# Kernel optimization log

Measured on AMD Instinct MI355X. Metric: run time of the kernel, lower is better.

Reference implementation:

```python
import jax, jax.numpy as jnp
import numpy as np

D_EMBED = 1024
N_HEADS = 16
D_HEAD = 64
D_MLP = 4096
SEQ = 2048
BATCH = 2
ALPHA = 1.0


def setup_inputs() -> dict:
    key = jax.random.key(0)
    ks = jax.random.split(key, 7)
    s = ALPHA / np.sqrt(D_EMBED)
    return {
        "x": jax.random.normal(ks[0], (BATCH, SEQ, D_EMBED), jnp.float32),
        "W_K": s * jax.random.normal(ks[1], (N_HEADS, D_HEAD, D_EMBED), jnp.float32),
        "W_Q": s * jax.random.normal(ks[2], (N_HEADS, D_HEAD, D_EMBED), jnp.float32),
        "W_V": s * jax.random.normal(ks[3], (N_HEADS, D_HEAD, D_EMBED), jnp.float32),
        "W_O": s * jax.random.normal(ks[4], (D_EMBED, N_HEADS * D_HEAD), jnp.float32),
        "W_in": s * jax.random.normal(ks[5], (D_MLP, D_EMBED), jnp.float32),
        "b_in": jnp.zeros((D_MLP,), jnp.float32),
        "W_out": s * jax.random.normal(ks[6], (D_EMBED, D_MLP), jnp.float32),
        "b_out": jnp.zeros((D_EMBED,), jnp.float32),
    }


def reference(x, W_K, W_Q, W_V, W_O, W_in, b_in, W_out, b_out):
    b, c_len, _ = x.shape
    d_head = W_K.shape[1]
    # q/k/v: [batch, head, ctx, d_head]
    k = jnp.einsum('ahe,bce->bach', W_K, x)
    q = jnp.einsum('ahe,bce->bach', W_Q, x)
    v = jnp.einsum('ahe,bce->bach', W_V, x)
    # scores[b,a,c,C] = k_c . q_C  (faithful to original index convention)
    scores = jnp.einsum('bach,baCh->bacC', k, q)
    mask = jnp.tril(jnp.ones((c_len, c_len), dtype=x.dtype))  # [c, C]
    masked = scores * mask - 1e10 * (1.0 - mask)
    attn = jax.nn.softmax(masked / np.sqrt(d_head), axis=-1)  # softmax over C (query idx)
    # z[b,a,C,h] = sum_c v[b,a,c,h] * attn[b,a,c,C]
    z = jnp.einsum('bach,bacC->baCh', v, attn)
    z_flat = jnp.transpose(z, (0, 2, 1, 3)).reshape(b, c_len, -1)  # [b, c, a*h]
    attn_out = jnp.einsum('ef,bcf->bce', W_O, z_flat)
    x = x + attn_out
    h = jnp.einsum('me,bce->bcm', W_in, x) + b_in
    h = jax.nn.relu(h)
    mlp_out = jnp.einsum('em,bcm->bce', W_out, h) + b_out
    return x + mlp_out
```

## Files before the change

kernel.cpp:

```cpp
#include <hip/hip_runtime.h>
#include <hip/hip_bf16.h>
#include <cstdint>
#include <cstddef>

typedef __bf16 bf16;
typedef bf16 bf16x4 __attribute__((ext_vector_type(4)));
typedef bf16 bf16x8 __attribute__((ext_vector_type(8)));
typedef float floatx4 __attribute__((ext_vector_type(4)));

#define MFMA16(a, b, c) __builtin_amdgcn_mfma_f32_16x16x32_bf16((a), (b), (c), 0, 0, 0)

#define K2 0.18033688011112042f

__device__ __forceinline__ void async16(const void* g, void* l) {
    __builtin_amdgcn_global_load_lds((const __attribute__((address_space(1))) void*)g,
                                     (__attribute__((address_space(3))) void*)l,
                                     16, 0, 0);
}

__device__ __forceinline__ void stage64s(const bf16* g0, int ldg, bf16* lds, int wave, int lane) {
#pragma unroll
    for (int i = 0; i < 2; ++i) {
        int r0 = wave * 16 + i * 8;
        async16(g0 + (size_t)(r0 + (lane >> 3)) * ldg + ((lane & 7) ^ (lane >> 3)) * 8,
                lds + r0 * 64);
    }
}
__device__ __forceinline__ bf16x8 rd64(const bf16* t, int row, int chunk) {
    return *(const bf16x8*)&t[row * 64 + ((chunk ^ (row & 7)) * 8)];
}
__device__ __forceinline__ bf16x8 rd32(const bf16* t, int row, int quad) {
    return *(const bf16x8*)&t[row * 32 + ((quad ^ (row & 3)) * 8)];
}

__global__ __launch_bounds__(256) void cvt_all(const float* __restrict__ x,
                                               const float* __restrict__ WQ,
                                               const float* __restrict__ WK,
                                               const float* __restrict__ WV,
                                               const float* __restrict__ WO,
                                               const float* __restrict__ Win,
                                               const float* __restrict__ Wout,
                                               bf16* __restrict__ xb,
                                               bf16* __restrict__ wqkv,
                                               bf16* __restrict__ wo,
                                               bf16* __restrict__ win,
                                               bf16* __restrict__ wout) {
    int blk = blockIdx.x;
    const float* src;
    bf16* dst;
    int off;
    if (blk < 1024)      { src = WQ;   dst = wqkv;           off = blk; }
    else if (blk < 2048) { src = WK;   dst = wqkv + 1048576; off = blk - 1024; }
    else if (blk < 3072) { src = WV;   dst = wqkv + 2097152; off = blk - 2048; }
    else if (blk < 4096) { src = WO;   dst = wo;             off = blk - 3072; }
    else if (blk < 8192) { src = Win;  dst = win;            off = blk - 4096; }
    else if (blk < 12288){ src = Wout; dst = wout;           off = blk - 8192; }
    else                 { src = x;    dst = xb;             off = blk - 12288; }
    int i = off * 1024 + threadIdx.x * 4;
    float4 v = *(const float4*)(src + i);
    bf16x4 o = {(bf16)v.x, (bf16)v.y, (bf16)v.z, (bf16)v.w};
    *(bf16x4*)(dst + i) = o;
}

template <int EPI, int NT>
__global__ __launch_bounds__(256) void gemm_pipe(const bf16* __restrict__ A, int lda,
                                                 const bf16* __restrict__ B, int ldb, int K,
                                                 float* __restrict__ Cf, bf16* __restrict__ Cb,
                                                 int ldc, const float* __restrict__ bias,
                                                 const float* __restrict__ res) {
    constexpr int NACC = NT / 32;
    __shared__ __align__(16) bf16 As[3][128 * 32];
    __shared__ __align__(16) bf16 Bs[3][NT * 32];
    const int tid = threadIdx.x, wave = tid >> 6, lane = tid & 63;
    const int m0 = blockIdx.y * 128, n0 = blockIdx.x * NT;
    const int wm = (wave >> 1) * 64, wn = (wave & 1) * (NT / 2);
    const int col = lane & 15, quad = lane >> 4;
    const int cs8 = ((lane & 3) ^ ((lane >> 2) & 3)) * 8;

    floatx4 acc[4][NACC];
#pragma unroll
    for (int mi = 0; mi < 4; ++mi)
#pragma unroll
        for (int ni = 0; ni < NACC; ++ni) acc[mi][ni] = (floatx4){0.f, 0.f, 0.f, 0.f};

    auto stage = [&](int buf, int k0) {
#pragma unroll
        for (int i = 0; i < 2; ++i) {
            int r0 = wave * 32 + i * 16;
            async16(A + (size_t)(m0 + r0 + (lane >> 2)) * lda + k0 + cs8,
                    As[buf] + r0 * 32);
        }
        if constexpr (NT == 128) {
#pragma unroll
            for (int i = 0; i < 2; ++i) {
                int r0 = wave * 32 + i * 16;
                async16(B + (size_t)(n0 + r0 + (lane >> 2)) * ldb + k0 + cs8,
                        Bs[buf] + r0 * 32);
            }
        } else {
            int r0 = wave * 16;
            async16(B + (size_t)(n0 + r0 + (lane >> 2)) * ldb + k0 + cs8,
                    Bs[buf] + r0 * 32);
        }
    };

    const int nk = K / 32;
    stage(0, 0);
    stage(1, 32);
    for (int it = 0; it < nk; ++it) {
        if (it + 1 < nk) {
            if constexpr (NT == 128) asm volatile("s_waitcnt vmcnt(4)" ::: "memory");
            else                     asm volatile("s_waitcnt vmcnt(3)" ::: "memory");
        } else {
            asm volatile("s_waitcnt vmcnt(0)" ::: "memory");
        }
        __builtin_amdgcn_s_barrier();
        if (it + 2 < nk) stage((it + 2) % 3, (it + 2) * 32);

        const bf16* as = As[it % 3];
        const bf16* bs = Bs[it % 3];
        bf16x8 af[4], bfr[NACC];
#pragma unroll
        for (int mi = 0; mi < 4; ++mi) af[mi] = rd32(as, wm + mi * 16 + col, quad);
#pragma unroll
        for (int ni = 0; ni < NACC; ++ni) bfr[ni] = rd32(bs, wn + ni * 16 + col, quad);
#pragma unroll
        for (int mi = 0; mi < 4; ++mi)
#pragma unroll
            for (int ni = 0; ni < NACC; ++ni)
                acc[mi][ni] = MFMA16(af[mi], bfr[ni], acc[mi][ni]);
    }

#pragma unroll
    for (int mi = 0; mi < 4; ++mi)
#pragma unroll
        for (int ni = 0; ni < NACC; ++ni)
#pragma unroll
            for (int r = 0; r < 4; ++r) {
                int row = m0 + wm + mi * 16 + quad * 4 + r;
                int cc = n0 + wn + ni * 16 + col;
                size_t idx = (size_t)row * ldc + cc;
                float v = acc[mi][ni][r];
                if constexpr (EPI == 0) {
                    Cb[idx] = (bf16)v;
                } else if constexpr (EPI == 1) {
                    v += res[idx];
                    Cf[idx] = v;
                    Cb[idx] = (bf16)v;
                } else if constexpr (EPI == 2) {
                    v += bias[cc];
                    v = fmaxf(v, 0.f);
                    Cb[idx] = (bf16)v;
                } else {
                    v += bias[cc] + Cf[idx];
                    Cf[idx] = v;
                }
            }
}

__global__ __launch_bounds__(256) void transpose_v(const bf16* __restrict__ qkv,
                                                   bf16* __restrict__ vt) {
    __shared__ bf16 t[64][65];
    const int bh = blockIdx.y, ct = blockIdx.x;
    const int b = bh >> 4, a = bh & 15;
    for (int idx = threadIdx.x; idx < 4096; idx += 256) {
        int c = idx >> 6, h = idx & 63;
        t[h][c] = qkv[(size_t)(b * 2048 + ct * 64 + c) * 3072 + 2048 + a * 64 + h];
    }
    __syncthreads();
    for (int idx = threadIdx.x; idx < 4096; idx += 256) {
        int h = idx >> 6, c = idx & 63;
        vt[(size_t)(bh * 64 + h) * 2048 + ct * 64 + c] = t[h][c];
    }
}

__global__ __launch_bounds__(256) void attn_stats(const bf16* __restrict__ qkv,
                                                  float* __restrict__ mp2) {
    __shared__ __align__(16) bf16 Kt[64 * 64];
    __shared__ __align__(16) bf16 Qt[3][64 * 64];
    const int xx = blockIdx.x;
    const int ct = (xx & 1) ? (31 - (xx >> 1)) : (xx >> 1);
    const int bh = blockIdx.y;
    const int b = bh >> 4, a = bh & 15;
    const int tid = threadIdx.x, wave = tid >> 6, lane = tid & 63;
    const int col = lane & 15, quad = lane >> 4;
    const bf16* base = qkv + (size_t)b * 2048 * 3072;

    stage64s(base + (size_t)ct * 64 * 3072 + 1024 + a * 64, 3072, Kt, wave, lane);
    stage64s(base + a * 64, 3072, Qt[0], wave, lane);
    if (ct >= 1) stage64s(base + (size_t)1 * 64 * 3072 + a * 64, 3072, Qt[1], wave, lane);

    float lrun[4] = {0.f, 0.f, 0.f, 0.f};
    bf16x8 a0, a1;

    for (int Ct = 0; Ct <= ct; ++Ct) {
        if (Ct < ct) asm volatile("s_waitcnt vmcnt(2)" ::: "memory");
        else         asm volatile("s_waitcnt vmcnt(0)" ::: "memory");
        __builtin_amdgcn_s_barrier();
        if (Ct + 2 <= ct)
            stage64s(base + (size_t)(Ct + 2) * 64 * 3072 + a * 64, 3072,
                     Qt[(Ct + 2) % 3], wave, lane);
        if (Ct == 0) {
            a0 = rd64(Kt, wave * 16 + col, quad);
            a1 = rd64(Kt, wave * 16 + col, quad + 4);
        }
        const bf16* q = Qt[Ct % 3];
#pragma unroll
        for (int nt = 0; nt < 4; ++nt) {
            bf16x8 b0 = rd64(q, nt * 16 + col, quad);
            bf16x8 b1 = rd64(q, nt * 16 + col, quad + 4);
            floatx4 sacc = (floatx4){0.f, 0.f, 0.f, 0.f};
            sacc = MFMA16(a0, b0, sacc);
            sacc = MFMA16(a1, b1, sacc);
#pragma unroll
            for (int r = 0; r < 4; ++r) {
                float e = __builtin_amdgcn_exp2f(sacc[r] * K2);
                if (Ct == ct && (nt * 16 + col) > (wave * 16 + quad * 4 + r)) e = 0.f;
                lrun[r] += e;
            }
        }
    }
#pragma unroll
    for (int r = 0; r < 4; ++r) {
        float t = lrun[r];
        t += __shfl_xor(t, 1);
        t += __shfl_xor(t, 2);
        t += __shfl_xor(t, 4);
        t += __shfl_xor(t, 8);
        lrun[r] = t;
    }
    if (col == 0) {
#pragma unroll
        for (int r = 0; r < 4; ++r) {
            int c = ct * 64 + wave * 16 + quad * 4 + r;
            mp2[(size_t)bh * 2048 + c] = __builtin_amdgcn_logf(lrun[r]);
        }
    }
}

__global__ __launch_bounds__(256) void attn_av(const bf16* __restrict__ qkv,
                                               const bf16* __restrict__ vt,
                                               const float* __restrict__ mp2,
                                               bf16* __restrict__ zb) {
    __shared__ __align__(16) bf16 Qt[64 * 64];
    __shared__ __align__(16) bf16 Kt[3][64 * 64];
    __shared__ __align__(16) bf16 Vt[3][64 * 64];
    __shared__ __align__(16) bf16 Pt[64 * 72];
    __shared__ __align__(16) float mpS[2048];
    const int xx = blockIdx.x;
    const int Ctile = (xx & 1) ? (31 - (xx >> 1)) : (xx >> 1);
    const int bh = blockIdx.y;
    const int b = bh >> 4, a = bh & 15;
    const int tid = threadIdx.x, wave = tid >> 6, lane = tid & 63;
    const int col = lane & 15, quad = lane >> 4;
    const bf16* base = qkv + (size_t)b * 2048 * 3072;
    const float* mpb = mp2 + (size_t)bh * 2048;
    const int niter = 32 - Ctile;

    stage64s(base + (size_t)Ctile * 64 * 3072 + a * 64, 3072, Qt, wave, lane);
    {
        int nb = niter * 256;
#pragma unroll
        for (int i = 0; i < 2; ++i) {
            int off = (i * 4 + wave) * 1024;
            if (off < nb)
                async16((const char*)(mpb + Ctile * 64) + off + lane * 16,
                        (char*)mpS + off);
        }
    }
    stage64s(base + (size_t)Ctile * 64 * 3072 + 1024 + a * 64, 3072, Kt[0], wave, lane);
    stage64s(vt + (size_t)bh * 64 * 2048 + Ctile * 64, 2048, Vt[0], wave, lane);
    if (niter > 1) {
        stage64s(base + (size_t)(Ctile + 1) * 64 * 3072 + 1024 + a * 64, 3072, Kt[1], wave, lane);
        stage64s(vt + (size_t)bh * 64 * 2048 + (Ctile + 1) * 64, 2048, Vt[1], wave, lane);
    }

    floatx4 zacc[4];
#pragma unroll
    for (int mi = 0; mi < 4; ++mi) zacc[mi] = (floatx4){0.f, 0.f, 0.f, 0.f};
    bf16x8 qf0[4], qf1[4];

    for (int i = 0; i < niter; ++i) {
        const int ct = Ctile + i;
        if (i + 1 < niter) asm volatile("s_waitcnt vmcnt(4)" ::: "memory");
        else               asm volatile("s_waitcnt vmcnt(0)" ::: "memory");
        __builtin_amdgcn_s_barrier();
        if (i + 2 < niter) {
            stage64s(base + (size_t)(ct + 2) * 64 * 3072 + 1024 + a * 64, 3072,
                     Kt[(i + 2) % 3], wave, lane);
            stage64s(vt + (size_t)bh * 64 * 2048 + (ct + 2) * 64, 2048,
                     Vt[(i + 2) % 3], wave, lane);
        }
        if (i == 0) {
#pragma unroll
            for (int nt = 0; nt < 4; ++nt) {
                qf0[nt] = rd64(Qt, nt * 16 + col, quad);
                qf1[nt] = rd64(Qt, nt * 16 + col, quad + 4);
            }
        }
        const bf16* kt = Kt[i % 3];
        const bf16* vts = Vt[i % 3];
        bf16x8 a0 = rd64(kt, wave * 16 + col, quad);
        bf16x8 a1 = rd64(kt, wave * 16 + col, quad + 4);
        float4 mpv = *(const float4*)&mpS[i * 64 + wave * 16 + quad * 4];
        const float mpl[4] = {mpv.x, mpv.y, mpv.z, mpv.w};

#pragma unroll
        for (int nt = 0; nt < 4; ++nt) {
            floatx4 sacc = (floatx4){0.f, 0.f, 0.f, 0.f};
            sacc = MFMA16(a0, qf0[nt], sacc);
            sacc = MFMA16(a1, qf1[nt], sacc);
            bf16x4 pv;
#pragma unroll
            for (int r = 0; r < 4; ++r) {
                float p;
                if (ct == Ctile && (nt * 16 + col) > (wave * 16 + quad * 4 + r))
                    p = 0.f;
                else
                    p = __builtin_amdgcn_exp2f(sacc[r] * K2 - mpl[r]);
                pv[r] = (bf16)p;
            }
            *(bf16x4*)&Pt[(nt * 16 + col) * 72 + wave * 16 + quad * 4] = pv;
        }
        asm volatile("s_waitcnt lgkmcnt(0)" ::: "memory");
        __builtin_amdgcn_s_barrier();

        bf16x8 v0 = rd64(vts, wave * 16 + col, quad);
        bf16x8 v1 = rd64(vts, wave * 16 + col, quad + 4);
#pragma unroll
        for (int mi = 0; mi < 4; ++mi) {
            bf16x8 p0 = *(const bf16x8*)&Pt[(mi * 16 + col) * 72 + quad * 8];
            bf16x8 p1 = *(const bf16x8*)&Pt[(mi * 16 + col) * 72 + 32 + quad * 8];
            zacc[mi] = MFMA16(p0, v0, zacc[mi]);
            zacc[mi] = MFMA16(p1, v1, zacc[mi]);
        }
    }
#pragma unroll
    for (int mi = 0; mi < 4; ++mi)
#pragma unroll
        for (int r = 0; r < 4; ++r) {
            int Cg = Ctile * 64 + mi * 16 + quad * 4 + r;
            zb[(size_t)(b * 2048 + Cg) * 1024 + a * 64 + wave * 16 + col] =
                (bf16)zacc[mi][r];
        }
}

extern "C" void kernel_launch(void* const* d_in, const int* in_sizes, int n_in,
                              void* d_out, int out_size, void* d_ws, size_t ws_size,
                              hipStream_t stream) {
    (void)in_sizes; (void)n_in; (void)out_size; (void)ws_size;
    const float* x    = (const float*)d_in[0];
    const float* WK   = (const float*)d_in[1];
    const float* WQ   = (const float*)d_in[2];
    const float* WV   = (const float*)d_in[3];
    const float* WO   = (const float*)d_in[4];
    const float* Win  = (const float*)d_in[5];
    const float* bin  = (const float*)d_in[6];
    const float* Wout = (const float*)d_in[7];
    const float* bout = (const float*)d_in[8];
    float* out = (float*)d_out;

    char* ws = (char*)d_ws;
    bf16*  xb   = (bf16*)(ws + 0);
    bf16*  wqkv = (bf16*)(ws + 8388608);
    bf16*  wo   = (bf16*)(ws + 14680064);
    bf16*  win  = (bf16*)(ws + 16777216);
    bf16*  wout = (bf16*)(ws + 25165824);
    bf16*  qkvb = (bf16*)(ws + 33554432);
    bf16*  vtb  = (bf16*)(ws + 58720256);
    float* mst  = (float*)(ws + 67108864);
    bf16*  zbuf = (bf16*)(ws + 67633152);
    bf16*  xmid = (bf16*)(ws + 76021760);
    bf16*  hbuf = (bf16*)(ws + 84410368);

    cvt_all<<<16384, 256, 0, stream>>>(x, WQ, WK, WV, WO, Win, Wout,
                                       xb, wqkv, wo, win, wout);

    gemm_pipe<0, 128><<<dim3(24, 32), 256, 0, stream>>>(xb, 1024, wqkv, 1024, 1024,
                                                        nullptr, qkvb, 3072, nullptr, nullptr);
    transpose_v<<<dim3(32, 32), 256, 0, stream>>>(qkvb, vtb);
    attn_stats<<<dim3(32, 32), 256, 0, stream>>>(qkvb, mst);
    attn_av<<<dim3(32, 32), 256, 0, stream>>>(qkvb, vtb, mst, zbuf);
    gemm_pipe<1, 64><<<dim3(16, 32), 256, 0, stream>>>(zbuf, 1024, wo, 1024, 1024,
                                                       out, xmid, 1024, nullptr, x);
    gemm_pipe<2, 128><<<dim3(32, 32), 256, 0, stream>>>(xmid, 1024, win, 1024, 1024,
                                                        nullptr, hbuf, 4096, bin, nullptr);
    gemm_pipe<3, 64><<<dim3(16, 32), 256, 0, stream>>>(hbuf, 4096, wout, 4096, 4096,
                                                       out, nullptr, 1024, bout, nullptr);
}
```

Measured before the change: 410.4 us.

## Replace triple-buffered GEMM pipeline with single-buffered K=64 tile loop

Rewrites the bf16 GEMM main loop so it no longer uses a three-stage async LDS pipeline with swizzled 32-wide K tiles. Each iteration now stages a 64-wide K tile into a single buffer, synchronises, and computes two MFMA substeps. This halves the number of barriers per K but removes the overlap of global loads with compute, and drops the XOR swizzle, which invites LDS bank conflicts. It may also rely on __syncthreads to drain the async LDS loads.

```diff
diff --git a/kernel.cpp b/kernel.cpp
--- a/kernel.cpp
+++ b/kernel.cpp
@@ -28,9 +28,6 @@
 }
 __device__ __forceinline__ bf16x8 rd64(const bf16* t, int row, int chunk) {
     return *(const bf16x8*)&t[row * 64 + ((chunk ^ (row & 7)) * 8)];
-}
-__device__ __forceinline__ bf16x8 rd32(const bf16* t, int row, int quad) {
-    return *(const bf16x8*)&t[row * 32 + ((quad ^ (row & 3)) * 8)];
 }
 
 __global__ __launch_bounds__(256) void cvt_all(const float* __restrict__ x,
@@ -63,19 +60,18 @@
 }
 
 template <int EPI, int NT>
-__global__ __launch_bounds__(256) void gemm_pipe(const bf16* __restrict__ A, int lda,
-                                                 const bf16* __restrict__ B, int ldb, int K,
-                                                 float* __restrict__ Cf, bf16* __restrict__ Cb,
-                                                 int ldc, const float* __restrict__ bias,
-                                                 const float* __restrict__ res) {
+__global__ __launch_bounds__(256) void gemm97(const bf16* __restrict__ A, int lda,
+                                              const bf16* __restrict__ B, int ldb, int K,
+                                              float* __restrict__ Cf, bf16* __restrict__ Cb,
+                                              int ldc, const float* __restrict__ bias,
+                                              const float* __restrict__ res) {
     constexpr int NACC = NT / 32;
-    __shared__ __align__(16) bf16 As[3][128 * 32];
-    __shared__ __align__(16) bf16 Bs[3][NT * 32];
+    __shared__ __align__(16) bf16 As[128 * 64];
+    __shared__ __align__(16) bf16 Bs[NT * 64];
     const int tid = threadIdx.x, wave = tid >> 6, lane = tid & 63;
     const int m0 = blockIdx.y * 128, n0 = blockIdx.x * NT;
     const int wm = (wave >> 1) * 64, wn = (wave & 1) * (NT / 2);
     const int col = lane & 15, quad = lane >> 4;
-    const int cs8 = ((lane & 3) ^ ((lane >> 2) & 3)) * 8;
 
     floatx4 acc[4][NACC];
 #pragma unroll
@@ -83,52 +79,45 @@
 #pragma unroll
         for (int ni = 0; ni < NACC; ++ni) acc[mi][ni] = (floatx4){0.f, 0.f, 0.f, 0.f};
 
-    auto stage = [&](int buf, int k0) {
-#pragma unroll
-        for (int i = 0; i < 2; ++i) {
-            int r0 = wave * 32 + i * 16;
-            async16(A + (size_t)(m0 + r0 + (lane >> 2)) * lda + k0 + cs8,
-                    As[buf] + r0 * 32);
+    const int rsub = lane >> 3, csub = (lane & 7) * 8;
+
+    for (int k0 = 0; k0 < K; k0 += 64) {
+        __syncthreads();
+#pragma unroll
+        for (int i = 0; i < 4; ++i) {
+            int r0 = wave * 32 + i * 8;
+            async16(A + (size_t)(m0 + r0 + rsub) * lda + k0 + csub, As + r0 * 64);
         }
         if constexpr (NT == 128) {
 #pragma unroll
+            for (int i = 0; i < 4; ++i) {
+                int r0 = wave * 32 + i * 8;
+                async16(B + (size_t)(n0 + r0 + rsub) * ldb + k0 + csub, Bs + r0 * 64);
+            }
+        } else {
+#pragma unroll
             for (int i = 0; i < 2; ++i) {
-                int r0 = wave * 32 + i * 16;
-                async16(B + (size_t)(n0 + r0 + (lane >> 2)) * ldb + k0 + cs8,
-                        Bs[buf] + r0 * 32);
-            }
-        } else {
-            int r0 = wave * 16;
-            async16(B + (size_t)(n0 + r0 + (lane >> 2)) * ldb + k0 + cs8,
-                    Bs[buf] + r0 * 32);
-        }
-    };
-
-    const int nk = K / 32;
-    stage(0, 0);
-    stage(1, 32);
-    for (int it = 0; it < nk; ++it) {
-        if (it + 1 < nk) {
-            if constexpr (NT == 128) asm volatile("s_waitcnt vmcnt(4)" ::: "memory");
-            else                     asm volatile("s_waitcnt vmcnt(3)" ::: "memory");
-        } else {
-            asm volatile("s_waitcnt vmcnt(0)" ::: "memory");
-        }
-        __builtin_amdgcn_s_barrier();
-        if (it + 2 < nk) stage((it + 2) % 3, (it + 2) * 32);
-
-        const bf16* as = As[it % 3];
-        const bf16* bs = Bs[it % 3];
-        bf16x8 af[4], bfr[NACC];
-#pragma unroll
-        for (int mi = 0; mi < 4; ++mi) af[mi] = rd32(as, wm + mi * 16 + col, quad);
-#pragma unroll
-        for (int ni = 0; ni < NACC; ++ni) bfr[ni] = rd32(bs, wn + ni * 16 + col, quad);
-#pragma unroll
-        for (int mi = 0; mi < 4; ++mi)
+                int r0 = wave * 16 + i * 8;
+                async16(B + (size_t)(n0 + r0 + rsub) * ldb + k0 + csub, Bs + r0 * 64);
+            }
+        }
+        __syncthreads();
+
+#pragma unroll
+        for (int ks = 0; ks < 2; ++ks) {
+            bf16x8 af[4], bfr[NACC];
+#pragma unroll
+            for (int mi = 0; mi < 4; ++mi)
+                af[mi] = *(const bf16x8*)&As[(wm + mi * 16 + col) * 64 + ks * 32 + quad * 8];
 #pragma unroll
             for (int ni = 0; ni < NACC; ++ni)
-                acc[mi][ni] = MFMA16(af[mi], bfr[ni], acc[mi][ni]);
+                bfr[ni] = *(const bf16x8*)&Bs[(wn + ni * 16 + col) * 64 + ks * 32 + quad * 8];
+#pragma unroll
+            for (int mi = 0; mi < 4; ++mi)
+#pragma unroll
+                for (int ni = 0; ni < NACC; ++ni)
+                    acc[mi][ni] = MFMA16(af[mi], bfr[ni], acc[mi][ni]);
+        }
     }
 
 #pragma unroll
@@ -376,15 +365,15 @@
     cvt_all<<<16384, 256, 0, stream>>>(x, WQ, WK, WV, WO, Win, Wout,
                                        xb, wqkv, wo, win, wout);
 
-    gemm_pipe<0, 128><<<dim3(24, 32), 256, 0, stream>>>(xb, 1024, wqkv, 1024, 1024,
-                                                        nullptr, qkvb, 3072, nullptr, nullptr);
+    gemm97<0, 128><<<dim3(24, 32), 256, 0, stream>>>(xb, 1024, wqkv, 1024, 1024,
+                                                     nullptr, qkvb, 3072, nullptr, nullptr);
     transpose_v<<<dim3(32, 32), 256, 0, stream>>>(qkvb, vtb);
     attn_stats<<<dim3(32, 32), 256, 0, stream>>>(qkvb, mst);
     attn_av<<<dim3(32, 32), 256, 0, stream>>>(qkvb, vtb, mst, zbuf);
-    gemm_pipe<1, 64><<<dim3(16, 32), 256, 0, stream>>>(zbuf, 1024, wo, 1024, 1024,
-                                                       out, xmid, 1024, nullptr, x);
-    gemm_pipe<2, 128><<<dim3(32, 32), 256, 0, stream>>>(xmid, 1024, win, 1024, 1024,
-                                                        nullptr, hbuf, 4096, bin, nullptr);
-    gemm_pipe<3, 64><<<dim3(16, 32), 256, 0, stream>>>(hbuf, 4096, wout, 4096, 4096,
-                                                       out, nullptr, 1024, bout, nullptr);
-}
+    gemm97<1, 64><<<dim3(16, 32), 256, 0, stream>>>(zbuf, 1024, wo, 1024, 1024,
+                                                    out, xmid, 1024, nullptr, x);
+    gemm97<2, 128><<<dim3(32, 32), 256, 0, stream>>>(xmid, 1024, win, 1024, 1024,
+                                                     nullptr, hbuf, 4096, bin, nullptr);
+    gemm97<3, 64><<<dim3(16, 32), 256, 0, stream>>>(hbuf, 4096, wout, 4096, 4096,
+                                                    out, nullptr, 1024, bout, nullptr);
+}
```

After: 424.6 us. +3.4%, slower.

## Add big-K-step GEMM kernel for the narrow output projections

Applied to the files above, without the earlier changes.

Adds a gemm_bigk kernel that stages 128-wide K slices of A and B into unswizzled LDS, with a barrier before and after each load and no multi-buffering. It is used for the W_O and W_out projections, which have N=1024. The 128-wide K step is meant to cut the number of barriers and loop iterations per tile. In exchange it drops the triple-buffered prefetch, so loads no longer overlap compute, and the unswizzled 256-byte LDS row stride likely causes bank conflicts on the fragment reads.

```diff
diff --git a/kernel.cpp b/kernel.cpp
--- a/kernel.cpp
+++ b/kernel.cpp
@@ -62,75 +62,11 @@
     *(bf16x4*)(dst + i) = o;
 }
 
-template <int EPI, int NT>
-__global__ __launch_bounds__(256) void gemm_pipe(const bf16* __restrict__ A, int lda,
-                                                 const bf16* __restrict__ B, int ldb, int K,
-                                                 float* __restrict__ Cf, bf16* __restrict__ Cb,
-                                                 int ldc, const float* __restrict__ bias,
-                                                 const float* __restrict__ res) {
-    constexpr int NACC = NT / 32;
-    __shared__ __align__(16) bf16 As[3][128 * 32];
-    __shared__ __align__(16) bf16 Bs[3][NT * 32];
-    const int tid = threadIdx.x, wave = tid >> 6, lane = tid & 63;
-    const int m0 = blockIdx.y * 128, n0 = blockIdx.x * NT;
-    const int wm = (wave >> 1) * 64, wn = (wave & 1) * (NT / 2);
-    const int col = lane & 15, quad = lane >> 4;
-    const int cs8 = ((lane & 3) ^ ((lane >> 2) & 3)) * 8;
-
-    floatx4 acc[4][NACC];
-#pragma unroll
-    for (int mi = 0; mi < 4; ++mi)
-#pragma unroll
-        for (int ni = 0; ni < NACC; ++ni) acc[mi][ni] = (floatx4){0.f, 0.f, 0.f, 0.f};
-
-    auto stage = [&](int buf, int k0) {
-#pragma unroll
-        for (int i = 0; i < 2; ++i) {
-            int r0 = wave * 32 + i * 16;
-            async16(A + (size_t)(m0 + r0 + (lane >> 2)) * lda + k0 + cs8,
-                    As[buf] + r0 * 32);
-        }
-        if constexpr (NT == 128) {
-#pragma unroll
-            for (int i = 0; i < 2; ++i) {
-                int r0 = wave * 32 + i * 16;
-                async16(B + (size_t)(n0 + r0 + (lane >> 2)) * ldb + k0 + cs8,
-                        Bs[buf] + r0 * 32);
-            }
-        } else {
-            int r0 = wave * 16;
-            async16(B + (size_t)(n0 + r0 + (lane >> 2)) * ldb + k0 + cs8,
-                    Bs[buf] + r0 * 32);
-        }
-    };
-
-    const int nk = K / 32;
-    stage(0, 0);
-    stage(1, 32);
-    for (int it = 0; it < nk; ++it) {
-        if (it + 1 < nk) {
-            if constexpr (NT == 128) asm volatile("s_waitcnt vmcnt(4)" ::: "memory");
-            else                     asm volatile("s_waitcnt vmcnt(3)" ::: "memory");
-        } else {
-            asm volatile("s_waitcnt vmcnt(0)" ::: "memory");
-        }
-        __builtin_amdgcn_s_barrier();
-        if (it + 2 < nk) stage((it + 2) % 3, (it + 2) * 32);
-
-        const bf16* as = As[it % 3];
-        const bf16* bs = Bs[it % 3];
-        bf16x8 af[4], bfr[NACC];
-#pragma unroll
-        for (int mi = 0; mi < 4; ++mi) af[mi] = rd32(as, wm + mi * 16 + col, quad);
-#pragma unroll
-        for (int ni = 0; ni < NACC; ++ni) bfr[ni] = rd32(bs, wn + ni * 16 + col, quad);
-#pragma unroll
-        for (int mi = 0; mi < 4; ++mi)
-#pragma unroll
-            for (int ni = 0; ni < NACC; ++ni)
-                acc[mi][ni] = MFMA16(af[mi], bfr[ni], acc[mi][ni]);
-    }
-
+template <int EPI, int NACC>
+__device__ __forceinline__ void epilogue(floatx4 (&acc)[4][NACC], int m0, int n0,
+                                         int wm, int wn, int col, int quad,
+                                         float* Cf, bf16* Cb, int ldc,
+                                         const float* bias, const float* res) {
 #pragma unroll
     for (int mi = 0; mi < 4; ++mi)
 #pragma unroll
@@ -158,6 +94,116 @@
             }
 }
 
+template <int EPI>
+__global__ __launch_bounds__(256) void gemm_pipe(const bf16* __restrict__ A, int lda,
+                                                 const bf16* __restrict__ B, int ldb, int K,
+                                                 float* __restrict__ Cf, bf16* __restrict__ Cb,
+                                                 int ldc, const float* __restrict__ bias,
+                                                 const float* __restrict__ res) {
+    __shared__ __align__(16) bf16 As[3][128 * 32];
+    __shared__ __align__(16) bf16 Bs[3][128 * 32];
+    const int tid = threadIdx.x, wave = tid >> 6, lane = tid & 63;
+    const int m0 = blockIdx.y * 128, n0 = blockIdx.x * 128;
+    const int wm = (wave >> 1) * 64, wn = (wave & 1) * 64;
+    const int col = lane & 15, quad = lane >> 4;
+    const int cs8 = ((lane & 3) ^ ((lane >> 2) & 3)) * 8;
+
+    floatx4 acc[4][4];
+#pragma unroll
+    for (int mi = 0; mi < 4; ++mi)
+#pragma unroll
+        for (int ni = 0; ni < 4; ++ni) acc[mi][ni] = (floatx4){0.f, 0.f, 0.f, 0.f};
+
+    auto stage = [&](int buf, int k0) {
+#pragma unroll
+        for (int i = 0; i < 2; ++i) {
+            int r0 = wave * 32 + i * 16;
+            async16(A + (size_t)(m0 + r0 + (lane >> 2)) * lda + k0 + cs8,
+                    As[buf] + r0 * 32);
+            async16(B + (size_t)(n0 + r0 + (lane >> 2)) * ldb + k0 + cs8,
+                    Bs[buf] + r0 * 32);
+        }
+    };
+
+    const int nk = K / 32;
+    stage(0, 0);
+    stage(1, 32);
+    for (int it = 0; it < nk; ++it) {
+        if (it + 1 < nk) asm volatile("s_waitcnt vmcnt(4)" ::: "memory");
+        else             asm volatile("s_waitcnt vmcnt(0)" ::: "memory");
+        __builtin_amdgcn_s_barrier();
+        if (it + 2 < nk) stage((it + 2) % 3, (it + 2) * 32);
+
+        const bf16* as = As[it % 3];
+        const bf16* bs = Bs[it % 3];
+        bf16x8 af[4], bfr[4];
+#pragma unroll
+        for (int mi = 0; mi < 4; ++mi) af[mi] = rd32(as, wm + mi * 16 + col, quad);
+#pragma unroll
+        for (int ni = 0; ni < 4; ++ni) bfr[ni] = rd32(bs, wn + ni * 16 + col, quad);
+#pragma unroll
+        for (int mi = 0; mi < 4; ++mi)
+#pragma unroll
+            for (int ni = 0; ni < 4; ++ni)
+                acc[mi][ni] = MFMA16(af[mi], bfr[ni], acc[mi][ni]);
+    }
+    epilogue<EPI, 4>(acc, m0, n0, wm, wn, col, quad, Cf, Cb, ldc, bias, res);
+}
+
+template <int EPI>
+__global__ __launch_bounds__(256) void gemm_bigk(const bf16* __restrict__ A, int lda,
+                                                 const bf16* __restrict__ B, int ldb, int K,
+                                                 float* __restrict__ Cf, bf16* __restrict__ Cb,
+                                                 int ldc, const float* __restrict__ bias,
+                                                 const float* __restrict__ res) {
+    __shared__ __align__(16) bf16 As[128 * 128];
+    __shared__ __align__(16) bf16 Bs[64 * 128];
+    const int tid = threadIdx.x, wave = tid >> 6, lane = tid & 63;
+    const int m0 = blockIdx.y * 128, n0 = blockIdx.x * 64;
+    const int wm = (wave >> 1) * 64, wn = (wave & 1) * 32;
+    const int col = lane & 15, quad = lane >> 4;
+
+    floatx4 acc[4][2];
+#pragma unroll
+    for (int mi = 0; mi < 4; ++mi)
+#pragma unroll
+        for (int ni = 0; ni < 2; ++ni) acc[mi][ni] = (floatx4){0.f, 0.f, 0.f, 0.f};
+
+    const int rsub = lane >> 4, csub = (lane & 15) * 8;
+
+    for (int k0 = 0; k0 < K; k0 += 128) {
+        __syncthreads();
+#pragma unroll
+        for (int i = 0; i < 8; ++i) {
+            int r0 = wave * 32 + i * 4;
+            async16(A + (size_t)(m0 + r0 + rsub) * lda + k0 + csub, As + r0 * 128);
+        }
+#pragma unroll
+        for (int i = 0; i < 4; ++i) {
+            int r0 = wave * 16 + i * 4;
+            async16(B + (size_t)(n0 + r0 + rsub) * ldb + k0 + csub, Bs + r0 * 128);
+        }
+        __syncthreads();
+
+#pragma unroll
+        for (int ks = 0; ks < 4; ++ks) {
+            bf16x8 af[4], bfr[2];
+#pragma unroll
+            for (int mi = 0; mi < 4; ++mi)
+                af[mi] = *(const bf16x8*)&As[(wm + mi * 16 + col) * 128 + ks * 32 + quad * 8];
+#pragma unroll
+            for (int ni = 0; ni < 2; ++ni)
+                bfr[ni] = *(const bf16x8*)&Bs[(wn + ni * 16 + col) * 128 + ks * 32 + quad * 8];
+#pragma unroll
+            for (int mi = 0; mi < 4; ++mi)
+#pragma unroll
+                for (int ni = 0; ni < 2; ++ni)
+                    acc[mi][ni] = MFMA16(af[mi], bfr[ni], acc[mi][ni]);
+        }
+    }
+    epilogue<EPI, 2>(acc, m0, n0, wm, wn, col, quad, Cf, Cb, ldc, bias, res);
+}
+
 __global__ __launch_bounds__(256) void transpose_v(const bf16* __restrict__ qkv,
                                                    bf16* __restrict__ vt) {
     __shared__ bf16 t[64][65];
@@ -376,15 +422,15 @@
     cvt_all<<<16384, 256, 0, stream>>>(x, WQ, WK, WV, WO, Win, Wout,
                                        xb, wqkv, wo, win, wout);
 
-    gemm_pipe<0, 128><<<dim3(24, 32), 256, 0, stream>>>(xb, 1024, wqkv, 1024, 1024,
-                                                        nullptr, qkvb, 3072, nullptr, nullptr);
+    gemm_pipe<0><<<dim3(24, 32), 256, 0, stream>>>(xb, 1024, wqkv, 1024, 1024,
+                                                   nullptr, qkvb, 3072, nullptr, nullptr);
     transpose_v<<<dim3(32, 32), 256, 0, stream>>>(qkvb, vtb);
     attn_stats<<<dim3(32, 32), 256, 0, stream>>>(qkvb, mst);
     attn_av<<<dim3(32, 32), 256, 0, stream>>>(qkvb, vtb, mst, zbuf);
-    gemm_pipe<1, 64><<<dim3(16, 32), 256, 0, stream>>>(zbuf, 1024, wo, 1024, 1024,
-                                                       out, xmid, 1024, nullptr, x);
-    gemm_pipe<2, 128><<<dim3(32, 32), 256, 0, stream>>>(xmid, 1024, win, 1024, 1024,
-                                                        nullptr, hbuf, 4096, bin, nullptr);
-    gemm_pipe<3, 64><<<dim3(16, 32), 256, 0, stream>>>(hbuf, 4096, wout, 4096, 4096,
-                                                       out, nullptr, 1024, bout, nullptr);
-}
+    gemm_bigk<1><<<dim3(16, 32), 256, 0, stream>>>(zbuf, 1024, wo, 1024, 1024,
+                                                   out, xmid, 1024, nullptr, x);
+    gemm_pipe<2><<<dim3(32, 32), 256, 0, stream>>>(xmid, 1024, win, 1024, 1024,
+                                                   nullptr, hbuf, 4096, bin, nullptr);
+    gemm_bigk<3><<<dim3(16, 32), 256, 0, stream>>>(hbuf, 4096, wout, 4096, 4096,
+                                                   out, nullptr, 1024, bout, nullptr);
+}
```

New measurement: 436.3 us. 1.06x slower.
